# Kernel optimization log

Hardware: AMD Instinct MI355X
Metric: run time of the kernel (lower is better)

## Reference

```python
import jax, jax.numpy as jnp
import numpy as np

B, C, H, W = 8, 256, 64, 64
C8 = C // 8


def setup_inputs() -> dict:
    key = jax.random.key(0)
    ks = jax.random.split(key, 8)
    scale = 0.05
    return {
        "x": jax.random.normal(ks[0], (B, C, H, W), jnp.float32),
        "Wf": jax.random.normal(ks[1], (C8, C), jnp.float32) * scale,
        "bf": jax.random.normal(ks[2], (C8,), jnp.float32) * scale,
        "Wg": jax.random.normal(ks[3], (C8, C), jnp.float32) * scale,
        "bg": jax.random.normal(ks[4], (C8,), jnp.float32) * scale,
        "Wh": jax.random.normal(ks[5], (C, C), jnp.float32) * scale,
        "bh": jax.random.normal(ks[6], (C,), jnp.float32) * scale,
        "gamma": jax.random.normal(ks[7], (1,), jnp.float32) * scale,
    }


def reference(x, Wf, bf, Wg, bg, Wh, bh, gamma):
    b, c, h, w = x.shape
    n = h * w
    xr = x.reshape(b, c, n)  # flatten spatial: [B, C, N]
    # 1x1 convs == per-pixel linear projections
    f = jnp.einsum('oc,bcn->bon', Wf, xr) + bf[None, :, None]  # [B, C/8, N]
    g = jnp.einsum('oc,bcn->bon', Wg, xr) + bg[None, :, None]  # [B, C/8, N]
    hh = jnp.einsum('oc,bcn->bon', Wh, xr) + bh[None, :, None]  # [B, C, N]
    # s = f^T @ g : unscaled attention logits, [B, N, N]
    s = jnp.einsum('bki,bkj->bij', f, g)
    attention = jax.nn.softmax(s, axis=-1)
    # out = h @ attention^T : out[b,c,i] = sum_j h[b,c,j] * attn[b,i,j]
    out = jnp.einsum('bcj,bij->bci', hh, attention)
    out = out.reshape(b, c, w, h)  # original code uses (W, H); H==W here
    out = gamma[0] * out + x
    return (out, attention)
```

## Files before the change

### kernel.cpp

```cpp
#include <hip/hip_runtime.h>
#include <hip/hip_bf16.h>

typedef unsigned short u16;
typedef __attribute__((ext_vector_type(8))) short short8;
typedef __attribute__((ext_vector_type(4))) float f32x4;

#define BATCH 8
#define CH 256
#define NPIX 4096
#define KD 32

static __device__ __forceinline__ u16 f2bf(float f) {
  union { __hip_bfloat16 h; u16 u; } cv;
  cv.h = __float2bfloat16(f);
  return cv.u;
}

__global__ __launch_bounds__(256) void proj_kernel(
    const float* __restrict__ x,
    const float* __restrict__ Wf, const float* __restrict__ bfp,
    const float* __restrict__ Wg, const float* __restrict__ bgp,
    const float* __restrict__ Wh, const float* __restrict__ bhp,
    u16* __restrict__ fT, u16* __restrict__ gT, u16* __restrict__ hhb)
{
  __shared__ float xs[CH][36];
  const int b  = blockIdx.x >> 7;
  const int n0 = (blockIdx.x & 127) * 32;
  const int t  = threadIdx.x;

  const float* xb = x + ((size_t)b * CH) * NPIX + n0;
  #pragma unroll
  for (int kk = 0; kk < 8; ++kk) {
    int v = kk * 256 + t;
    int c = v >> 3, p4 = v & 7;
    float4 d = *(const float4*)(xb + (size_t)c * NPIX + p4 * 4);
    *(float4*)&xs[c][p4 * 4] = d;
  }
  __syncthreads();

  const int o = t;
  float acch[32];
  #pragma unroll
  for (int p = 0; p < 32; ++p) acch[p] = bhp[o];

  const int o2 = t & 63;
  const int oo = o2 & 31;
  const bool isf = o2 < 32;
  const float* Wfg = isf ? Wf : Wg;
  const float bias2 = isf ? bfp[oo] : bgp[oo];
  const int pg = (t >> 6) * 8;
  float accf[8];
  #pragma unroll
  for (int p = 0; p < 8; ++p) accf[p] = bias2;

  const float* whr  = Wh  + o * CH;
  const float* wfgr = Wfg + oo * CH;
  for (int c = 0; c < CH; c += 4) {
    float4 wh4 = *(const float4*)(whr + c);
    float4 wf4 = *(const float4*)(wfgr + c);
    float wha[4] = {wh4.x, wh4.y, wh4.z, wh4.w};
    float wfa[4] = {wf4.x, wf4.y, wf4.z, wf4.w};
    #pragma unroll
    for (int cc = 0; cc < 4; ++cc) {
      float wh = wha[cc], wf = wfa[cc];
      #pragma unroll
      for (int p4 = 0; p4 < 8; ++p4) {
        float4 xv = *(const float4*)&xs[c + cc][p4 * 4];
        acch[p4*4+0] = fmaf(wh, xv.x, acch[p4*4+0]);
        acch[p4*4+1] = fmaf(wh, xv.y, acch[p4*4+1]);
        acch[p4*4+2] = fmaf(wh, xv.z, acch[p4*4+2]);
        acch[p4*4+3] = fmaf(wh, xv.w, acch[p4*4+3]);
      }
      #pragma unroll
      for (int p = 0; p < 8; ++p) accf[p] = fmaf(wf, xs[c + cc][pg + p], accf[p]);
    }
  }

  u16* hrow = hhb + ((size_t)b * CH + o) * NPIX + n0;
  #pragma unroll
  for (int q = 0; q < 4; ++q) {
    uint4 u;
    u.x = f2bf(acch[q*8+0]) | ((unsigned)f2bf(acch[q*8+1]) << 16);
    u.y = f2bf(acch[q*8+2]) | ((unsigned)f2bf(acch[q*8+3]) << 16);
    u.z = f2bf(acch[q*8+4]) | ((unsigned)f2bf(acch[q*8+5]) << 16);
    u.w = f2bf(acch[q*8+6]) | ((unsigned)f2bf(acch[q*8+7]) << 16);
    *(uint4*)(hrow + q * 8) = u;
  }
  u16* dst = (isf ? fT : gT) + ((size_t)b * NPIX + n0 + pg) * KD + oo;
  #pragma unroll
  for (int p = 0; p < 8; ++p) dst[(size_t)p * KD] = f2bf(accf[p]);
}

__global__ __launch_bounds__(512, 2) void fused_attn_pv(
    const u16* __restrict__ fT, const u16* __restrict__ gT,
    const u16* __restrict__ hhb, const float* __restrict__ x,
    const float* __restrict__ gamma,
    float* __restrict__ attn_out, float* __restrict__ outp)
{
  __shared__ u16 Pt[2][64 * 64];
  __shared__ float part[8][64];
  __shared__ float invs[64];

  const int bid = blockIdx.x;
  const int b  = bid & 7;
  const int n0 = (bid >> 3) * 64;
  const int t  = threadIdx.x;
  const int iw = t >> 6, l = t & 63;
  const int lg = l >> 4, lm = l & 15;

  const u16* fb = fT + ((size_t)b * NPIX + n0) * KD;
  const u16* gb = gT + (size_t)b * NPIX * KD;
  const u16* hb = hhb + (size_t)b * CH * NPIX;

  f32x4 z4 = {0.f, 0.f, 0.f, 0.f};

  short8 ff[4];
  #pragma unroll
  for (int it = 0; it < 4; ++it)
    ff[it] = *(const short8*)(fb + (it * 16 + lm) * KD + lg * 8);

  float sum[4][4];
  #pragma unroll
  for (int it = 0; it < 4; ++it)
    #pragma unroll
    for (int r = 0; r < 4; ++r) sum[it][r] = 0.f;

  const int j1 = iw * 512;
  for (int jt = 0; jt < 32; ++jt) {
    int j0 = j1 + jt * 16;
    short8 gf = *(const short8*)(gb + (size_t)(j0 + lm) * KD + lg * 8);
    #pragma unroll
    for (int it = 0; it < 4; ++it) {
      f32x4 s = __builtin_amdgcn_mfma_f32_16x16x32_bf16(ff[it], gf, z4, 0, 0, 0);
      #pragma unroll
      for (int r = 0; r < 4; ++r) sum[it][r] += __expf(s[r]);
    }
  }
  #pragma unroll
  for (int m = 1; m < 16; m <<= 1)
    #pragma unroll
    for (int it = 0; it < 4; ++it)
      #pragma unroll
      for (int r = 0; r < 4; ++r) sum[it][r] += __shfl_xor(sum[it][r], m, 64);
  if (lm == 0) {
    #pragma unroll
    for (int it = 0; it < 4; ++it)
      #pragma unroll
      for (int r = 0; r < 4; ++r) part[iw][it * 16 + lg * 4 + r] = sum[it][r];
  }
  __syncthreads();
  if (t < 64) {
    float s = 0.f;
    #pragma unroll
    for (int w2 = 0; w2 < 8; ++w2) s += part[w2][t];
    invs[t] = 1.0f / s;
  }
  __syncthreads();

  const int it2 = iw >> 1, jsub = iw & 1;
  float inv4[4];
  #pragma unroll
  for (int r = 0; r < 4; ++r) inv4[r] = invs[it2 * 16 + lg * 4 + r];
  const short8 f2 = ff[it2];

  float* arow = attn_out + ((size_t)b * NPIX + n0 + it2 * 16 + lg * 4) * NPIX;

  f32x4 acc[2][4];
  #pragma unroll
  for (int mf = 0; mf < 2; ++mf)
    #pragma unroll
    for (int nf = 0; nf < 4; ++nf) acc[mf][nf] = z4;

  short8 gP[2], gQ[2];

  auto LDG = [&](short8 (&g2)[2], int JC) {
    #pragma unroll
    for (int st = 0; st < 2; ++st)
      g2[st] = *(const short8*)(gb + (size_t)(JC + jsub * 32 + st * 16 + lm) * KD + lg * 8);
  };

  auto HALF = [&](u16* buf, short8 (&gc)[2], short8 (&gn)[2], int JC, int JN) {
    f32x4 s[2];
    #pragma unroll
    for (int st = 0; st < 2; ++st)
      s[st] = __builtin_amdgcn_mfma_f32_16x16x32_bf16(f2, gc[st], z4, 0, 0, 0);
    LDG(gn, JN);
    short8 hc[2][2];
    #pragma unroll
    for (int m = 0; m < 2; ++m)
      #pragma unroll
      for (int ks = 0; ks < 2; ++ks)
        hc[m][ks] = *(const short8*)(hb + (size_t)(iw * 32 + m * 16 + lm) * NPIX
                                     + JC + ks * 32 + lg * 8);
    #pragma unroll
    for (int st = 0; st < 2; ++st) {
      const int j0 = JC + jsub * 32 + st * 16;
      #pragma unroll
      for (int r = 0; r < 4; ++r) {
        float p = __expf(s[st][r]) * inv4[r];
        __builtin_nontemporal_store(p, arow + (size_t)r * NPIX + j0 + lm);
        int iloc = it2 * 16 + lg * 4 + r;
        int jloc = jsub * 32 + st * 16 + lm;
        int byte = iloc * 128 + ((jloc * 2) ^ (((lg * 4 + r) & 7) << 4));
        *(u16*)((char*)buf + byte) = f2bf(p);
      }
    }
    asm volatile("s_waitcnt lgkmcnt(0)\n\ts_barrier" ::: "memory");
    #pragma unroll
    for (int nf = 0; nf < 4; ++nf) {
      #pragma unroll
      for (int ks = 0; ks < 2; ++ks) {
        int byte = (nf * 16 + lm) * 128 + (((ks * 4 + lg) * 16) ^ ((lm & 7) << 4));
        short8 pf = *(const short8*)((char*)buf + byte);
        acc[0][nf] = __builtin_amdgcn_mfma_f32_16x16x32_bf16(hc[0][ks], pf, acc[0][nf], 0, 0, 0);
        acc[1][nf] = __builtin_amdgcn_mfma_f32_16x16x32_bf16(hc[1][ks], pf, acc[1][nf], 0, 0, 0);
      }
    }
  };

  LDG(gP, 0);
  for (int jc = 0; jc < NPIX; jc += 128) {
    int n1 = (jc + 64) & (NPIX - 1);
    int n2 = (jc + 128) & (NPIX - 1);
    HALF(&Pt[0][0], gP, gQ, jc, n1);
    HALF(&Pt[1][0], gQ, gP, jc + 64, n2);
  }

  const float gm = gamma[0];
  #pragma unroll
  for (int mf = 0; mf < 2; ++mf) {
    #pragma unroll
    for (int r = 0; r < 4; ++r) {
      int c = iw * 32 + mf * 16 + lg * 4 + r;
      #pragma unroll
      for (int nf = 0; nf < 4; ++nf) {
        int i = n0 + nf * 16 + lm;
        size_t idx = ((size_t)b * CH + c) * NPIX + i;
        outp[idx] = fmaf(gm, acc[mf][nf][r], x[idx]);
      }
    }
  }
}

extern "C" void kernel_launch(void* const* d_in, const int* in_sizes, int n_in,
                              void* d_out, int out_size, void* d_ws, size_t ws_size,
                              hipStream_t stream) {
  const float* x     = (const float*)d_in[0];
  const float* Wf    = (const float*)d_in[1];
  const float* bf    = (const float*)d_in[2];
  const float* Wg    = (const float*)d_in[3];
  const float* bg    = (const float*)d_in[4];
  const float* Wh    = (const float*)d_in[5];
  const float* bh    = (const float*)d_in[6];
  const float* gamma = (const float*)d_in[7];

  float* outp = (float*)d_out;
  float* attn_out = outp + (size_t)BATCH * CH * NPIX;

  u16* fT = (u16*)d_ws;
  u16* gT = fT + (size_t)BATCH * NPIX * KD;
  u16* hh = gT + (size_t)BATCH * NPIX * KD;

  proj_kernel<<<dim3(BATCH * (NPIX / 32)), dim3(256), 0, stream>>>(
      x, Wf, bf, Wg, bg, Wh, bh, fT, gT, hh);

  fused_attn_pv<<<dim3(BATCH * (NPIX / 64)), dim3(512), 0, stream>>>(
      fT, gT, hh, x, gamma, attn_out, outp);
}
```

Baseline: 346.3 us.

## Stage attention output through LDS for coalesced 16-byte nontemporal stores

The attention matrix is no longer written with scattered scalar fp32 stores straight from MFMA registers. Each thread now reads back an 8-element row segment of the bf16 probability tile already held in shared memory, widens it to fp32 and writes it with two 16-byte nontemporal stores, so the 512 MB attention write becomes coalesced. It also raises the launch-bounds occupancy hint from 2 to 4 blocks and raises wave priority around the PV MFMA loop. The attention output now carries only bf16 precision, and the tighter register budget risks spills.

```diff
diff --git a/kernel.cpp b/kernel.cpp
--- a/kernel.cpp
+++ b/kernel.cpp
@@ -14,6 +14,12 @@
   union { __hip_bfloat16 h; u16 u; } cv;
   cv.h = __float2bfloat16(f);
   return cv.u;
+}
+
+static __device__ __forceinline__ float bf2f(u16 u) {
+  union { unsigned int i; float f; } cv;
+  cv.i = ((unsigned int)u) << 16;
+  return cv.f;
 }
 
 __global__ __launch_bounds__(256) void proj_kernel(
@@ -91,7 +97,7 @@
   for (int p = 0; p < 8; ++p) dst[(size_t)p * KD] = f2bf(accf[p]);
 }
 
-__global__ __launch_bounds__(512, 2) void fused_attn_pv(
+__global__ __launch_bounds__(512, 4) void fused_attn_pv(
     const u16* __restrict__ fT, const u16* __restrict__ gT,
     const u16* __restrict__ hhb, const float* __restrict__ x,
     const float* __restrict__ gamma,
@@ -163,7 +169,10 @@
   for (int r = 0; r < 4; ++r) inv4[r] = invs[it2 * 16 + lg * 4 + r];
   const short8 f2 = ff[it2];
 
-  float* arow = attn_out + ((size_t)b * NPIX + n0 + it2 * 16 + lg * 4) * NPIX;
+  float* abase = attn_out + ((size_t)b * NPIX + n0) * NPIX;
+  const int srow = t >> 3;
+  const int scol = (t & 7) * 8;
+  const int rdbyte = srow * 128 + ((scol * 2) ^ ((srow & 7) << 4));
 
   f32x4 acc[2][4];
   #pragma unroll
@@ -180,10 +189,8 @@
   };
 
   auto HALF = [&](u16* buf, short8 (&gc)[2], short8 (&gn)[2], int JC, int JN) {
-    f32x4 s[2];
-    #pragma unroll
-    for (int st = 0; st < 2; ++st)
-      s[st] = __builtin_amdgcn_mfma_f32_16x16x32_bf16(f2, gc[st], z4, 0, 0, 0);
+    f32x4 s0 = __builtin_amdgcn_mfma_f32_16x16x32_bf16(f2, gc[0], z4, 0, 0, 0);
+    f32x4 s1 = __builtin_amdgcn_mfma_f32_16x16x32_bf16(f2, gc[1], z4, 0, 0, 0);
     LDG(gn, JN);
     short8 hc[2][2];
     #pragma unroll
@@ -192,30 +199,37 @@
       for (int ks = 0; ks < 2; ++ks)
         hc[m][ks] = *(const short8*)(hb + (size_t)(iw * 32 + m * 16 + lm) * NPIX
                                      + JC + ks * 32 + lg * 8);
-    #pragma unroll
-    for (int st = 0; st < 2; ++st) {
-      const int j0 = JC + jsub * 32 + st * 16;
-      #pragma unroll
-      for (int r = 0; r < 4; ++r) {
-        float p = __expf(s[st][r]) * inv4[r];
-        __builtin_nontemporal_store(p, arow + (size_t)r * NPIX + j0 + lm);
-        int iloc = it2 * 16 + lg * 4 + r;
-        int jloc = jsub * 32 + st * 16 + lm;
-        int byte = iloc * 128 + ((jloc * 2) ^ (((lg * 4 + r) & 7) << 4));
-        *(u16*)((char*)buf + byte) = f2bf(p);
-      }
+    const int ibyte = (it2 * 16 + lg * 4) * 128;
+    #pragma unroll
+    for (int r = 0; r < 4; ++r) {
+      float p0 = __expf(s0[r]) * inv4[r];
+      float p1 = __expf(s1[r]) * inv4[r];
+      int row = ibyte + r * 128;
+      int sw  = ((lg * 4 + r) & 7) << 4;
+      int j0  = (jsub * 32 + lm) * 2;
+      *(u16*)((char*)buf + row + (j0 ^ sw)) = f2bf(p0);
+      *(u16*)((char*)buf + row + ((j0 + 32) ^ sw)) = f2bf(p1);
     }
     asm volatile("s_waitcnt lgkmcnt(0)\n\ts_barrier" ::: "memory");
+    __builtin_amdgcn_s_setprio(1);
     #pragma unroll
     for (int nf = 0; nf < 4; ++nf) {
       #pragma unroll
       for (int ks = 0; ks < 2; ++ks) {
         int byte = (nf * 16 + lm) * 128 + (((ks * 4 + lg) * 16) ^ ((lm & 7) << 4));
-        short8 pf = *(const short8*)((char*)buf + byte);
-        acc[0][nf] = __builtin_amdgcn_mfma_f32_16x16x32_bf16(hc[0][ks], pf, acc[0][nf], 0, 0, 0);
-        acc[1][nf] = __builtin_amdgcn_mfma_f32_16x16x32_bf16(hc[1][ks], pf, acc[1][nf], 0, 0, 0);
+        short8 pfr = *(const short8*)((char*)buf + byte);
+        acc[0][nf] = __builtin_amdgcn_mfma_f32_16x16x32_bf16(hc[0][ks], pfr, acc[0][nf], 0, 0, 0);
+        acc[1][nf] = __builtin_amdgcn_mfma_f32_16x16x32_bf16(hc[1][ks], pfr, acc[1][nf], 0, 0, 0);
       }
     }
+    __builtin_amdgcn_s_setprio(0);
+    short8 pw = *(const short8*)((char*)buf + rdbyte);
+    f32x4 o0, o1;
+    #pragma unroll
+    for (int q = 0; q < 4; ++q) { o0[q] = bf2f((u16)pw[q]); o1[q] = bf2f((u16)pw[q + 4]); }
+    float* dst = abase + (size_t)srow * NPIX + JC + scol;
+    __builtin_nontemporal_store(o0, (f32x4*)dst);
+    __builtin_nontemporal_store(o1, (f32x4*)(dst + 4));
   };
 
   LDG(gP, 0);
```

New measurement: 360.0 us. 4.0% more time.
